# Optimization experiments

Hardware: AMD Instinct MI355X
Metric: run time of the kernel (lower is better)

## Reference

```python
import jax, jax.numpy as jnp
import numpy as np

N = 50000      # nodes
F_IN = 128     # input features
H = 128        # hidden channels
C = 2          # num classes
E = 1600000    # edges
EPS = 1e-5     # BatchNorm eps


def setup_inputs() -> dict:
    key = jax.random.key(0)
    ks = jax.random.split(key, 4)
    x = jax.random.normal(ks[0], (N, F_IN), dtype=jnp.float32)
    edge_index = jax.random.randint(ks[1], (2, E), 0, N, dtype=jnp.int64)
    W1 = jax.random.normal(ks[2], (F_IN, H), dtype=jnp.float32) * 0.05
    W2 = jax.random.normal(ks[3], (H, C), dtype=jnp.float32) * 0.05
    return {
        "x": x, "edge_index": edge_index,
        "bn0_gamma": jnp.ones((F_IN,), jnp.float32), "bn0_beta": jnp.zeros((F_IN,), jnp.float32),
        "bn0_mean": jnp.zeros((F_IN,), jnp.float32), "bn0_var": jnp.ones((F_IN,), jnp.float32),
        "W1": W1, "b1": jnp.zeros((H,), jnp.float32),
        "bn1_gamma": jnp.ones((H,), jnp.float32), "bn1_beta": jnp.zeros((H,), jnp.float32),
        "bn1_mean": jnp.zeros((H,), jnp.float32), "bn1_var": jnp.ones((H,), jnp.float32),
        "W2": W2, "b2": jnp.zeros((C,), jnp.float32),
    }


def batch_norm_eval(x, gamma, beta, mean, var):
    # BatchNorm over nodes, eval mode: use running stats
    return (x - mean) * jax.lax.rsqrt(var + EPS) * gamma + beta


def gcn_conv(x, edge_index, W, b):
    # GCNConv: x @ W, add self-loops, symmetric deg^{-1/2} normalization, scatter-add
    n = x.shape[0]
    xw = x @ W  # [N, out]
    loop = jnp.arange(n, dtype=edge_index.dtype)
    src = jnp.concatenate([edge_index[0], loop])
    dst = jnp.concatenate([edge_index[1], loop])
    deg = jax.ops.segment_sum(jnp.ones_like(dst, dtype=x.dtype), dst, num_segments=n)
    dinv = jnp.where(deg > 0, jax.lax.rsqrt(jnp.maximum(deg, 1.0)), 0.0)
    norm = dinv[src] * dinv[dst]  # [E+N]
    out = jax.ops.segment_sum(xw[src] * norm[:, None], dst, num_segments=n)
    return out + b


def reference(x, edge_index, bn0_gamma, bn0_beta, bn0_mean, bn0_var,
              W1, b1, bn1_gamma, bn1_beta, bn1_mean, bn1_var, W2, b2):
    # Eval mode: dropout / dropout_edge are identity
    h = batch_norm_eval(x, bn0_gamma, bn0_beta, bn0_mean, bn0_var)
    h = gcn_conv(h, edge_index, W1, b1)
    h = batch_norm_eval(h, bn1_gamma, bn1_beta, bn1_mean, bn1_var)
    h = jax.nn.relu(h)
    return gcn_conv(h, edge_index, W2, b2)
```

## Files before the change

### kernel.cpp

```cpp
#include <hip/hip_runtime.h>

#define EPS 1e-5f
#define CAP 128
#define DR  128
#define NB  391
#define CB  4608
#define GS  16
#define CHUNK 4096

typedef __attribute__((ext_vector_type(8))) short bf16x8;
typedef __attribute__((ext_vector_type(4))) float f32x4;

__device__ __forceinline__ unsigned int f2bf(float f) {
  union { float f; unsigned int u; } v; v.f = f;
  return (v.u + 0x7fffu + ((v.u >> 16) & 1u)) >> 16;
}
__device__ __forceinline__ float bf2f_lo(unsigned int u) {
  union { unsigned int i; float f; } v; v.i = u << 16; return v.f;
}
__device__ __forceinline__ float bf2f_hi(unsigned int u) {
  union { unsigned int i; float f; } v; v.i = u & 0xffff0000u; return v.f;
}

__global__ __launch_bounds__(256) void k_prep0(const float* __restrict__ W1, const float* __restrict__ b1,
                       const float* __restrict__ g0, const float* __restrict__ be0,
                       const float* __restrict__ m0, const float* __restrict__ v0,
                       const float* __restrict__ g1, const float* __restrict__ be1,
                       const float* __restrict__ m1, const float* __restrict__ v1,
                       float* __restrict__ W1p, float* __restrict__ c1,
                       float* __restrict__ s1, float* __restrict__ u1,
                       int* __restrict__ gcur) {
  if (blockIdx.x > 0) {
    int i = (blockIdx.x - 1) * 256 + threadIdx.x;
    if (i < NB * GS) gcur[i] = 0;
    return;
  }
  int j = threadIdx.x;
  if (j >= 128) return;
  float acc = 0.f;
  for (int k = 0; k < 128; ++k) {
    float s0 = g0[k] * rsqrtf(v0[k] + EPS);
    float t0 = be0[k] - m0[k] * s0;
    float w = W1[k * 128 + j];
    W1p[k * 128 + j] = s0 * w;
    acc = fmaf(t0, w, acc);
  }
  c1[j] = acc;
  float s = g1[j] * rsqrtf(v1[j] + EPS);
  s1[j] = s;
  u1[j] = fmaf(b1[j] - m1[j], s, be1[j]);
}

__global__ __launch_bounds__(256) void k_cvtx(const float4* __restrict__ x,
                                              uint2* __restrict__ Xb4,
                                              int n4, int npad4) {
  int i = blockIdx.x * 256 + threadIdx.x;
  if (i >= npad4) return;
  uint2 o = make_uint2(0u, 0u);
  if (i < n4) {
    float4 v = x[i];
    o.x = (f2bf(v.y) << 16) | f2bf(v.x);
    o.y = (f2bf(v.w) << 16) | f2bf(v.z);
  }
  Xb4[i] = o;
}

__global__ __launch_bounds__(256) void k_p1(const int* __restrict__ esrc,
                                            const int* __restrict__ edst,
                                            int* __restrict__ gcur,
                                            uint2* __restrict__ coarse, int e) {
  __shared__ int hist[NB];
  __shared__ int base[NB];
  __shared__ int loff[NB];
  for (int i = threadIdx.x; i < NB; i += 256) { hist[i] = 0; loff[i] = 0; }
  __syncthreads();
  int e0 = blockIdx.x * CHUNK;
  int e1 = min(e0 + CHUNK, e);
  for (int i = e0 + threadIdx.x; i < e1; i += 256)
    atomicAdd(&hist[edst[i] >> 7], 1);
  __syncthreads();
  for (int b = threadIdx.x; b < NB; b += 256) {
    int h = hist[b];
    if (h > 0) base[b] = atomicAdd(&gcur[b * GS], h);
  }
  __syncthreads();
  for (int i = e0 + threadIdx.x; i < e1; i += 256) {
    int d = edst[i], s = esrc[i];
    int b = d >> 7;
    int p = base[b] + atomicAdd(&loff[b], 1);
    if (p < CB) coarse[(size_t)b * CB + p] = make_uint2((uint)s, (uint)d);
  }
}

__global__ __launch_bounds__(256) void k_p2(const int* __restrict__ gcur,
                                            const uint2* __restrict__ coarse,
                                            int* __restrict__ slot,
                                            int* __restrict__ wcnt,
                                            float* __restrict__ dinv, int n) {
  __shared__ int lcnt[DR];
  __shared__ int nqs[DR];
  __shared__ int lslot[DR * CAP];
  for (int i = threadIdx.x; i < DR; i += 256) lcnt[i] = 0;
  for (int q = threadIdx.x; q < DR * CAP; q += 256) lslot[q] = n;
  __syncthreads();
  int cb = blockIdx.x;
  int cnt = gcur[cb * GS]; if (cnt > CB) cnt = CB;
  const uint2* src = coarse + (size_t)cb * CB;
  for (int i = threadIdx.x; i < cnt; i += 256) {
    uint2 pr = src[i];
    int ld = (int)(pr.y & 127u);
    int pos = atomicAdd(&lcnt[ld], 1);
    if (pos < CAP) lslot[ld * CAP + pos] = (int)pr.x;
  }
  __syncthreads();
  int dbase = cb * DR;
  for (int ld = threadIdx.x; ld < DR; ld += 256) {
    int c = min(lcnt[ld], CAP);
    nqs[ld] = (c + 3) >> 2;
    int d = dbase + ld;
    if (d < n) {
      wcnt[d] = c;
      dinv[d] = rsqrtf((float)c + 1.0f);
    }
  }
  __syncthreads();
  const int4* lslot4 = (const int4*)lslot;
  int4* slot4 = (int4*)slot;
  for (int idx = threadIdx.x; idx < DR * 32; idx += 256) {
    int ld = idx >> 5, qi = idx & 31;
    if (qi < nqs[ld]) slot4[(size_t)cb * (DR * 32) + idx] = lslot4[idx];
  }
}

__global__ __launch_bounds__(256) void k_gemm1m(const unsigned short* __restrict__ Xb,
                                                const float* __restrict__ W1p,
                                                const float* __restrict__ c1,
                                                const float* __restrict__ dinv,
                                                unsigned short* __restrict__ xsb, int n) {
  __shared__ short wsw[32 * 64 * 8];
  __shared__ float c1s[128];
  const int tid = threadIdx.x;
  for (int idx = tid; idx < 128 * 32; idx += 256) {
    int k = idx >> 5, n4 = (idx & 31) * 4;
    float4 w = ((const float4*)W1p)[idx];
    int c = k >> 5, j = k & 7, lq2 = (k >> 3) & 3;
    float wv[4] = {w.x, w.y, w.z, w.w};
#pragma unroll
    for (int m = 0; m < 4; ++m) {
      int col = n4 + m;
      int t = col >> 4, li = col & 15;
      int l = lq2 * 16 + li;
      wsw[(((c << 3) + t) * 64 + l) * 8 + j] = (short)f2bf(wv[m]);
    }
  }
  if (tid < 128) c1s[tid] = c1[tid];
  if (blockIdx.x == 0 && tid < 16)
    ((uint4*)xsb)[(size_t)n * 16 + tid] = make_uint4(0, 0, 0, 0);
  __syncthreads();
  const int wave = tid >> 6, lane = tid & 63;
  const int r0 = blockIdx.x * 64 + wave * 16;
  const int lr = lane & 15, lq = lane >> 4;
  const bf16x8* a_base = (const bf16x8*)(Xb + (size_t)(r0 + lr) * 128);
  f32x4 acc[8];
#pragma unroll
  for (int t = 0; t < 8; ++t) acc[t] = (f32x4){0.f, 0.f, 0.f, 0.f};
#pragma unroll
  for (int c = 0; c < 4; ++c) {
    bf16x8 a = a_base[c * 4 + lq];
    const bf16x8* bbase = (const bf16x8*)wsw + (c * 8) * 64 + lane;
#pragma unroll
    for (int t = 0; t < 8; ++t) {
      bf16x8 b = bbase[t * 64];
      acc[t] = __builtin_amdgcn_mfma_f32_16x16x32_bf16(a, b, acc[t], 0, 0, 0);
    }
  }
#pragma unroll
  for (int reg = 0; reg < 4; ++reg) {
    int row = r0 + lq * 4 + reg;
    if (row < n) {
      float dd = dinv[row];
      unsigned short* orow = xsb + (size_t)row * 128 + lr;
#pragma unroll
      for (int t = 0; t < 8; ++t) {
        float v = (acc[t][reg] + c1s[t * 16 + lr]) * dd;
        orow[t * 16] = (unsigned short)f2bf(v);
      }
    }
  }
}

__global__ __launch_bounds__(256) void k_gather1(const int* __restrict__ wcnt,
                                                 const int* __restrict__ slot,
                                                 const uint4* __restrict__ xs4,
                                                 const float* __restrict__ dinv,
                                                 const float* __restrict__ s1,
                                                 const float* __restrict__ u1,
                                                 const float* __restrict__ W2,
                                                 float* __restrict__ xs2, int n) {
  int wave = threadIdx.x >> 6, lane = threadIdx.x & 63;
  int d = blockIdx.x * 4 + wave;
  if (d >= n) return;
  int sub = lane >> 4, cl = lane & 15;
  int cnt = wcnt[d];
  int nq = (cnt + 3) >> 2;
  const int* slotd = slot + ((size_t)d << 7);
  float a0 = 0.f, a1 = 0.f, a2 = 0.f, a3 = 0.f, a4 = 0.f, a5 = 0.f, a6 = 0.f, a7 = 0.f;
#define ACC(R) { a0 += bf2f_lo(R.x); a1 += bf2f_hi(R.x); a2 += bf2f_lo(R.y); a3 += bf2f_hi(R.y); \
                 a4 += bf2f_lo(R.z); a5 += bf2f_hi(R.z); a6 += bf2f_lo(R.w); a7 += bf2f_hi(R.w); }
  int q = 0;
  for (; q + 1 < nq; q += 2) {
    int i0 = slotd[q * 4 + sub];
    int i1 = slotd[q * 4 + 4 + sub];
    uint4 r0 = xs4[(size_t)i0 * 16 + cl];
    uint4 r1 = xs4[(size_t)i1 * 16 + cl];
    ACC(r0); ACC(r1);
  }
  if (q < nq) {
    int i0 = slotd[q * 4 + sub];
    uint4 r0 = xs4[(size_t)i0 * 16 + cl];
    ACC(r0);
  }
#define FOLD(OFF) { a0 += __shfl_xor(a0, OFF); a1 += __shfl_xor(a1, OFF); \
                    a2 += __shfl_xor(a2, OFF); a3 += __shfl_xor(a3, OFF); \
                    a4 += __shfl_xor(a4, OFF); a5 += __shfl_xor(a5, OFF); \
                    a6 += __shfl_xor(a6, OFF); a7 += __shfl_xor(a7, OFF); }
  FOLD(16); FOLD(32);
  uint4 sr = xs4[(size_t)d * 16 + cl];
  ACC(sr);
#undef ACC
#undef FOLD
  float dd = dinv[d];
  float4 sA = ((const float4*)s1)[cl * 2], sB = ((const float4*)s1)[cl * 2 + 1];
  float4 uA = ((const float4*)u1)[cl * 2], uB = ((const float4*)u1)[cl * 2 + 1];
  float h0 = fmaxf(fmaf(a0 * dd, sA.x, uA.x), 0.f);
  float h1 = fmaxf(fmaf(a1 * dd, sA.y, uA.y), 0.f);
  float h2 = fmaxf(fmaf(a2 * dd, sA.z, uA.z), 0.f);
  float h3 = fmaxf(fmaf(a3 * dd, sA.w, uA.w), 0.f);
  float h4 = fmaxf(fmaf(a4 * dd, sB.x, uB.x), 0.f);
  float h5 = fmaxf(fmaf(a5 * dd, sB.y, uB.y), 0.f);
  float h6 = fmaxf(fmaf(a6 * dd, sB.z, uB.z), 0.f);
  float h7 = fmaxf(fmaf(a7 * dd, sB.w, uB.w), 0.f);
  float4 wA = ((const float4*)W2)[cl * 4 + 0];
  float4 wB = ((const float4*)W2)[cl * 4 + 1];
  float4 wC = ((const float4*)W2)[cl * 4 + 2];
  float4 wD = ((const float4*)W2)[cl * 4 + 3];
  float p0 = h0 * wA.x + h1 * wA.z + h2 * wB.x + h3 * wB.z
           + h4 * wC.x + h5 * wC.z + h6 * wD.x + h7 * wD.z;
  float p1 = h0 * wA.y + h1 * wA.w + h2 * wB.y + h3 * wB.w
           + h4 * wC.y + h5 * wC.w + h6 * wD.y + h7 * wD.w;
  for (int off = 1; off < 16; off <<= 1) {
    p0 += __shfl_xor(p0, off);
    p1 += __shfl_xor(p1, off);
  }
  if (lane == 0) ((float2*)xs2)[d] = make_float2(p0 * dd, p1 * dd);
}

__global__ __launch_bounds__(256) void k_gather2(const int* __restrict__ wcnt,
                                                 const int* __restrict__ slot,
                                                 const float* __restrict__ xs2,
                                                 const float* __restrict__ dinv,
                                                 const float* __restrict__ b2,
                                                 float* __restrict__ out, int n) {
  int wave = threadIdx.x >> 6, lane = threadIdx.x & 63;
  int d = blockIdx.x * 4 + wave;
  if (d >= n) return;
  int cnt = wcnt[d];
  const int* slotd = slot + ((size_t)d << 7);
  float p0 = 0.f, p1 = 0.f;
  for (int k = lane; k < cnt; k += 64) {
    int s = slotd[k];
    float2 v = ((const float2*)xs2)[s];
    p0 += v.x; p1 += v.y;
  }
  for (int off = 32; off > 0; off >>= 1) {
    p0 += __shfl_down(p0, off);
    p1 += __shfl_down(p1, off);
  }
  if (lane == 0) {
    float dd = dinv[d];
    float2 self = ((const float2*)xs2)[d];
    out[d * 2 + 0] = fmaf(dd, p0 + self.x, b2[0]);
    out[d * 2 + 1] = fmaf(dd, p1 + self.y, b2[1]);
  }
}

extern "C" void kernel_launch(void* const* d_in, const int* in_sizes, int n_in,
                              void* d_out, int out_size, void* d_ws, size_t ws_size,
                              hipStream_t stream) {
  const float* x   = (const float*)d_in[0];
  const int*   ei  = (const int*)d_in[1];
  const float* g0  = (const float*)d_in[2];
  const float* be0 = (const float*)d_in[3];
  const float* m0  = (const float*)d_in[4];
  const float* v0  = (const float*)d_in[5];
  const float* W1  = (const float*)d_in[6];
  const float* b1  = (const float*)d_in[7];
  const float* g1  = (const float*)d_in[8];
  const float* be1 = (const float*)d_in[9];
  const float* m1  = (const float*)d_in[10];
  const float* v1  = (const float*)d_in[11];
  const float* W2  = (const float*)d_in[12];
  const float* b2  = (const float*)d_in[13];
  float* out = (float*)d_out;

  const int n = in_sizes[0] / 128;
  const int e = in_sizes[1] / 2;
  const int* esrc = ei;
  const int* edst = ei + e;
  const int npad = ((n + 63) / 64) * 64;

  int*   gcur   = (int*)d_ws;
  uint2* coarse = (uint2*)(gcur + 6272);
  int*   slot   = (int*)(coarse + (size_t)NB * CB);
  int*   wcnt   = slot + (size_t)n * CAP;
  float* dinv   = (float*)(wcnt + n);
  float* W1p    = dinv + n;
  float* c1     = W1p + 128 * 128;
  float* s1     = c1 + 128;
  float* u1     = s1 + 128;
  float* xs2    = u1 + 128;
  unsigned short* Xb = (unsigned short*)(xs2 + (size_t)n * 2);
  unsigned short* xsb = (unsigned short*)coarse;

  k_prep0<<<1 + (NB * GS + 255) / 256, 256, 0, stream>>>(W1, b1, g0, be0, m0, v0, g1, be1, m1, v1,
                                                         W1p, c1, s1, u1, gcur);
  k_cvtx<<<(npad * 32 + 255) / 256, 256, 0, stream>>>((const float4*)x, (uint2*)Xb,
                                                      n * 32, npad * 32);
  k_p1<<<(e + CHUNK - 1) / CHUNK, 256, 0, stream>>>(esrc, edst, gcur, coarse, e);
  k_p2<<<NB, 256, 0, stream>>>(gcur, coarse, slot, wcnt, dinv, n);
  k_gemm1m<<<npad / 64, 256, 0, stream>>>(Xb, W1p, c1, dinv, xsb, n);
  k_gather1<<<(n + 3) / 4, 256, 0, stream>>>(wcnt, slot, (const uint4*)xsb, dinv, s1, u1, W2, xs2, n);
  k_gather2<<<(n + 3) / 4, 256, 0, stream>>>(wcnt, slot, xs2, dinv, b2, out, n);
}
```

Before: 243.2 us.

## Pack edge/slot indices to 16-bit, fuse prep kernels, preswizzle W1 once

```diff
diff --git a/kernel.cpp b/kernel.cpp
--- a/kernel.cpp
+++ b/kernel.cpp
@@ -7,6 +7,7 @@
 #define CB  4608
 #define GS  16
 #define CHUNK 4096
+#define GZB ((NB * GS + 255) / 256)
 
 typedef __attribute__((ext_vector_type(8))) short bf16x8;
 typedef __attribute__((ext_vector_type(4))) float f32x4;
@@ -22,39 +23,51 @@
   union { unsigned int i; float f; } v; v.i = u & 0xffff0000u; return v.f;
 }
 
-__global__ __launch_bounds__(256) void k_prep0(const float* __restrict__ W1, const float* __restrict__ b1,
-                       const float* __restrict__ g0, const float* __restrict__ be0,
-                       const float* __restrict__ m0, const float* __restrict__ v0,
-                       const float* __restrict__ g1, const float* __restrict__ be1,
-                       const float* __restrict__ m1, const float* __restrict__ v1,
-                       float* __restrict__ W1p, float* __restrict__ c1,
-                       float* __restrict__ s1, float* __restrict__ u1,
-                       int* __restrict__ gcur) {
-  if (blockIdx.x > 0) {
-    int i = (blockIdx.x - 1) * 256 + threadIdx.x;
+__global__ __launch_bounds__(256) void k_prep_all(
+    const float* __restrict__ W1, const float* __restrict__ b1,
+    const float* __restrict__ g0, const float* __restrict__ be0,
+    const float* __restrict__ m0, const float* __restrict__ v0,
+    const float* __restrict__ g1, const float* __restrict__ be1,
+    const float* __restrict__ m1, const float* __restrict__ v1,
+    const float4* __restrict__ x,
+    unsigned short* __restrict__ Wb, float* __restrict__ c1,
+    float* __restrict__ s1, float* __restrict__ u1,
+    int* __restrict__ gcur, uint2* __restrict__ Xb4, int n4, int npad4) {
+  int bid = blockIdx.x;
+  int tid = threadIdx.x;
+  if (bid == 0) {
+    __shared__ float s0s[128], t0s[128];
+    if (tid < 128) {
+      float s0 = g0[tid] * rsqrtf(v0[tid] + EPS);
+      s0s[tid] = s0;
+      t0s[tid] = be0[tid] - m0[tid] * s0;
+      float s = g1[tid] * rsqrtf(v1[tid] + EPS);
+      s1[tid] = s;
+      u1[tid] = fmaf(b1[tid] - m1[tid], s, be1[tid]);
+    }
+    __syncthreads();
+    if (tid < 128) {
+      float acc = 0.f;
+      for (int k = 0; k < 128; ++k) acc = fmaf(t0s[k], W1[k * 128 + tid], acc);
+      c1[tid] = acc;
+    }
+    for (int idx = tid; idx < 16384; idx += 256) {
+      int k = idx >> 7, col = idx & 127;
+      float w = W1[idx] * s0s[k];
+      int c = k >> 5, j = k & 7, lq2 = (k >> 3) & 3;
+      int t = col >> 4, li = col & 15;
+      Wb[(((c * 8 + t) * 64) + lq2 * 16 + li) * 8 + j] = (unsigned short)f2bf(w);
+    }
+    return;
+  }
+  bid -= 1;
+  if (bid < GZB) {
+    int i = bid * 256 + tid;
     if (i < NB * GS) gcur[i] = 0;
     return;
   }
-  int j = threadIdx.x;
-  if (j >= 128) return;
-  float acc = 0.f;
-  for (int k = 0; k < 128; ++k) {
-    float s0 = g0[k] * rsqrtf(v0[k] + EPS);
-    float t0 = be0[k] - m0[k] * s0;
-    float w = W1[k * 128 + j];
-    W1p[k * 128 + j] = s0 * w;
-    acc = fmaf(t0, w, acc);
-  }
-  c1[j] = acc;
-  float s = g1[j] * rsqrtf(v1[j] + EPS);
-  s1[j] = s;
-  u1[j] = fmaf(b1[j] - m1[j], s, be1[j]);
-}
-
-__global__ __launch_bounds__(256) void k_cvtx(const float4* __restrict__ x,
-                                              uint2* __restrict__ Xb4,
-                                              int n4, int npad4) {
-  int i = blockIdx.x * 256 + threadIdx.x;
+  bid -= GZB;
+  int i = bid * 256 + tid;
   if (i >= npad4) return;
   uint2 o = make_uint2(0u, 0u);
   if (i < n4) {
@@ -68,7 +81,7 @@
 __global__ __launch_bounds__(256) void k_p1(const int* __restrict__ esrc,
                                             const int* __restrict__ edst,
                                             int* __restrict__ gcur,
-                                            uint2* __restrict__ coarse, int e) {
+                                            unsigned int* __restrict__ coarse, int e) {
   __shared__ int hist[NB];
   __shared__ int base[NB];
   __shared__ int loff[NB];
@@ -79,7 +92,9 @@
   for (int i = e0 + threadIdx.x; i < e1; i += 256)
     atomicAdd(&hist[edst[i] >> 7], 1);
   __syncthreads();
-  for (int b = threadIdx.x; b < NB; b += 256) {
+  int rot = blockIdx.x % NB;
+  for (int bb = threadIdx.x; bb < NB; bb += 256) {
+    int b = bb + rot; if (b >= NB) b -= NB;
     int h = hist[b];
     if (h > 0) base[b] = atomicAdd(&gcur[b * GS], h);
   }
@@ -88,35 +103,36 @@
     int d = edst[i], s = esrc[i];
     int b = d >> 7;
     int p = base[b] + atomicAdd(&loff[b], 1);
-    if (p < CB) coarse[(size_t)b * CB + p] = make_uint2((uint)s, (uint)d);
+    if (p < CB) coarse[(size_t)b * CB + p] = ((unsigned int)(d & 127) << 16) | (unsigned int)s;
   }
 }
 
 __global__ __launch_bounds__(256) void k_p2(const int* __restrict__ gcur,
-                                            const uint2* __restrict__ coarse,
-                                            int* __restrict__ slot,
+                                            const unsigned int* __restrict__ coarse,
+                                            unsigned short* __restrict__ slot,
                                             int* __restrict__ wcnt,
                                             float* __restrict__ dinv, int n) {
   __shared__ int lcnt[DR];
-  __shared__ int nqs[DR];
-  __shared__ int lslot[DR * CAP];
+  __shared__ int nqr[DR];
+  __shared__ unsigned short lslot[DR * CAP];
   for (int i = threadIdx.x; i < DR; i += 256) lcnt[i] = 0;
-  for (int q = threadIdx.x; q < DR * CAP; q += 256) lslot[q] = n;
+  unsigned int padpat = ((unsigned int)n << 16) | (unsigned int)n;
+  for (int q = threadIdx.x; q < DR * CAP / 2; q += 256) ((unsigned int*)lslot)[q] = padpat;
   __syncthreads();
   int cb = blockIdx.x;
   int cnt = gcur[cb * GS]; if (cnt > CB) cnt = CB;
-  const uint2* src = coarse + (size_t)cb * CB;
+  const unsigned int* src = coarse + (size_t)cb * CB;
   for (int i = threadIdx.x; i < cnt; i += 256) {
-    uint2 pr = src[i];
-    int ld = (int)(pr.y & 127u);
+    unsigned int v = src[i];
+    int ld = (int)(v >> 16);
     int pos = atomicAdd(&lcnt[ld], 1);
-    if (pos < CAP) lslot[ld * CAP + pos] = (int)pr.x;
+    if (pos < CAP) lslot[ld * CAP + pos] = (unsigned short)(v & 0xffffu);
   }
   __syncthreads();
   int dbase = cb * DR;
   for (int ld = threadIdx.x; ld < DR; ld += 256) {
     int c = min(lcnt[ld], CAP);
-    nqs[ld] = (c + 3) >> 2;
+    nqr[ld] = ((((c + 3) >> 2) + 3) & ~3);
     int d = dbase + ld;
     if (d < n) {
       wcnt[d] = c;
@@ -124,53 +140,36 @@
     }
   }
   __syncthreads();
-  const int4* lslot4 = (const int4*)lslot;
-  int4* slot4 = (int4*)slot;
+  const uint2* ls8 = (const uint2*)lslot;
+  uint2* s8 = (uint2*)slot;
   for (int idx = threadIdx.x; idx < DR * 32; idx += 256) {
     int ld = idx >> 5, qi = idx & 31;
-    if (qi < nqs[ld]) slot4[(size_t)cb * (DR * 32) + idx] = lslot4[idx];
+    if (qi < nqr[ld] && dbase + ld < n) s8[(size_t)cb * (DR * 32) + idx] = ls8[idx];
   }
 }
 
 __global__ __launch_bounds__(256) void k_gemm1m(const unsigned short* __restrict__ Xb,
-                                                const float* __restrict__ W1p,
+                                                const unsigned short* __restrict__ Wb,
                                                 const float* __restrict__ c1,
                                                 const float* __restrict__ dinv,
                                                 unsigned short* __restrict__ xsb, int n) {
-  __shared__ short wsw[32 * 64 * 8];
-  __shared__ float c1s[128];
   const int tid = threadIdx.x;
-  for (int idx = tid; idx < 128 * 32; idx += 256) {
-    int k = idx >> 5, n4 = (idx & 31) * 4;
-    float4 w = ((const float4*)W1p)[idx];
-    int c = k >> 5, j = k & 7, lq2 = (k >> 3) & 3;
-    float wv[4] = {w.x, w.y, w.z, w.w};
-#pragma unroll
-    for (int m = 0; m < 4; ++m) {
-      int col = n4 + m;
-      int t = col >> 4, li = col & 15;
-      int l = lq2 * 16 + li;
-      wsw[(((c << 3) + t) * 64 + l) * 8 + j] = (short)f2bf(wv[m]);
-    }
-  }
-  if (tid < 128) c1s[tid] = c1[tid];
   if (blockIdx.x == 0 && tid < 16)
     ((uint4*)xsb)[(size_t)n * 16 + tid] = make_uint4(0, 0, 0, 0);
-  __syncthreads();
   const int wave = tid >> 6, lane = tid & 63;
   const int r0 = blockIdx.x * 64 + wave * 16;
   const int lr = lane & 15, lq = lane >> 4;
   const bf16x8* a_base = (const bf16x8*)(Xb + (size_t)(r0 + lr) * 128);
+  const bf16x8* wb = (const bf16x8*)Wb;
   f32x4 acc[8];
 #pragma unroll
   for (int t = 0; t < 8; ++t) acc[t] = (f32x4){0.f, 0.f, 0.f, 0.f};
 #pragma unroll
   for (int c = 0; c < 4; ++c) {
     bf16x8 a = a_base[c * 4 + lq];
-    const bf16x8* bbase = (const bf16x8*)wsw + (c * 8) * 64 + lane;
 #pragma unroll
     for (int t = 0; t < 8; ++t) {
-      bf16x8 b = bbase[t * 64];
+      bf16x8 b = wb[(c * 8 + t) * 64 + lane];
       acc[t] = __builtin_amdgcn_mfma_f32_16x16x32_bf16(a, b, acc[t], 0, 0, 0);
     }
   }
@@ -182,7 +181,7 @@
       unsigned short* orow = xsb + (size_t)row * 128 + lr;
 #pragma unroll
       for (int t = 0; t < 8; ++t) {
-        float v = (acc[t][reg] + c1s[t * 16 + lr]) * dd;
+        float v = (acc[t][reg] + c1[t * 16 + lr]) * dd;
         orow[t * 16] = (unsigned short)f2bf(v);
       }
     }
@@ -190,7 +189,7 @@
 }
 
 __global__ __launch_bounds__(256) void k_gather1(const int* __restrict__ wcnt,
-                                                 const int* __restrict__ slot,
+                                                 const unsigned short* __restrict__ slot,
                                                  const uint4* __restrict__ xs4,
                                                  const float* __restrict__ dinv,
                                                  const float* __restrict__ s1,
@@ -202,23 +201,21 @@
   if (d >= n) return;
   int sub = lane >> 4, cl = lane & 15;
   int cnt = wcnt[d];
-  int nq = (cnt + 3) >> 2;
-  const int* slotd = slot + ((size_t)d << 7);
+  int nq4 = ((((cnt + 3) >> 2) + 3) & ~3);
+  const unsigned short* slotd = slot + ((size_t)d << 7);
   float a0 = 0.f, a1 = 0.f, a2 = 0.f, a3 = 0.f, a4 = 0.f, a5 = 0.f, a6 = 0.f, a7 = 0.f;
 #define ACC(R) { a0 += bf2f_lo(R.x); a1 += bf2f_hi(R.x); a2 += bf2f_lo(R.y); a3 += bf2f_hi(R.y); \
                  a4 += bf2f_lo(R.z); a5 += bf2f_hi(R.z); a6 += bf2f_lo(R.w); a7 += bf2f_hi(R.w); }
-  int q = 0;
-  for (; q + 1 < nq; q += 2) {
-    int i0 = slotd[q * 4 + sub];
-    int i1 = slotd[q * 4 + 4 + sub];
+  for (int q = 0; q < nq4; q += 4) {
+    int i0 = slotd[(q + 0) * 4 + sub];
+    int i1 = slotd[(q + 1) * 4 + sub];
+    int i2 = slotd[(q + 2) * 4 + sub];
+    int i3 = slotd[(q + 3) * 4 + sub];
     uint4 r0 = xs4[(size_t)i0 * 16 + cl];
     uint4 r1 = xs4[(size_t)i1 * 16 + cl];
-    ACC(r0); ACC(r1);
-  }
-  if (q < nq) {
-    int i0 = slotd[q * 4 + sub];
-    uint4 r0 = xs4[(size_t)i0 * 16 + cl];
-    ACC(r0);
+    uint4 r2 = xs4[(size_t)i2 * 16 + cl];
+    uint4 r3 = xs4[(size_t)i3 * 16 + cl];
+    ACC(r0); ACC(r1); ACC(r2); ACC(r3);
   }
 #define FOLD(OFF) { a0 += __shfl_xor(a0, OFF); a1 += __shfl_xor(a1, OFF); \
                     a2 += __shfl_xor(a2, OFF); a3 += __shfl_xor(a3, OFF); \
@@ -256,7 +253,7 @@
 }
 
 __global__ __launch_bounds__(256) void k_gather2(const int* __restrict__ wcnt,
-                                                 const int* __restrict__ slot,
+                                                 const unsigned short* __restrict__ slot,
                                                  const float* __restrict__ xs2,
                                                  const float* __restrict__ dinv,
                                                  const float* __restrict__ b2,
@@ -265,7 +262,7 @@
   int d = blockIdx.x * 4 + wave;
   if (d >= n) return;
   int cnt = wcnt[d];
-  const int* slotd = slot + ((size_t)d << 7);
+  const unsigned short* slotd = slot + ((size_t)d << 7);
   float p0 = 0.f, p1 = 0.f;
   for (int k = lane; k < cnt; k += 64) {
     int s = slotd[k];
@@ -309,26 +306,26 @@
   const int* edst = ei + e;
   const int npad = ((n + 63) / 64) * 64;
 
-  int*   gcur   = (int*)d_ws;
-  uint2* coarse = (uint2*)(gcur + 6272);
-  int*   slot   = (int*)(coarse + (size_t)NB * CB);
-  int*   wcnt   = slot + (size_t)n * CAP;
-  float* dinv   = (float*)(wcnt + n);
-  float* W1p    = dinv + n;
-  float* c1     = W1p + 128 * 128;
-  float* s1     = c1 + 128;
-  float* u1     = s1 + 128;
-  float* xs2    = u1 + 128;
-  unsigned short* Xb = (unsigned short*)(xs2 + (size_t)n * 2);
-  unsigned short* xsb = (unsigned short*)coarse;
-
-  k_prep0<<<1 + (NB * GS + 255) / 256, 256, 0, stream>>>(W1, b1, g0, be0, m0, v0, g1, be1, m1, v1,
-                                                         W1p, c1, s1, u1, gcur);
-  k_cvtx<<<(npad * 32 + 255) / 256, 256, 0, stream>>>((const float4*)x, (uint2*)Xb,
-                                                      n * 32, npad * 32);
+  int*            gcur   = (int*)d_ws;
+  unsigned int*   coarse = (unsigned int*)(gcur + 6272);
+  unsigned short* slot   = (unsigned short*)(coarse + (size_t)NB * CB);
+  int*            wcnt   = (int*)(slot + (size_t)n * CAP);
+  float*          dinv   = (float*)(wcnt + n);
+  unsigned short* Wb     = (unsigned short*)(dinv + n);
+  float*          c1     = (float*)(Wb + 16384);
+  float*          s1     = c1 + 128;
+  float*          u1     = s1 + 128;
+  float*          xs2    = u1 + 128;
+  unsigned short* Xb     = (unsigned short*)(xs2 + (size_t)n * 2);
+  unsigned short* xsb    = Xb + (size_t)npad * 128;
+
+  const int cvb = (npad * 32 + 255) / 256;
+  k_prep_all<<<1 + GZB + cvb, 256, 0, stream>>>(W1, b1, g0, be0, m0, v0, g1, be1, m1, v1,
+                                                (const float4*)x, Wb, c1, s1, u1, gcur,
+                                                (uint2*)Xb, n * 32, npad * 32);
   k_p1<<<(e + CHUNK - 1) / CHUNK, 256, 0, stream>>>(esrc, edst, gcur, coarse, e);
   k_p2<<<NB, 256, 0, stream>>>(gcur, coarse, slot, wcnt, dinv, n);
-  k_gemm1m<<<npad / 64, 256, 0, stream>>>(Xb, W1p, c1, dinv, xsb, n);
+  k_gemm1m<<<npad / 64, 256, 0, stream>>>(Xb, Wb, c1, dinv, xsb, n);
   k_gather1<<<(n + 3) / 4, 256, 0, stream>>>(wcnt, slot, (const uint4*)xsb, dinv, s1, u1, W2, xs2, n);
   k_gather2<<<(n + 3) / 4, 256, 0, stream>>>(wcnt, slot, xs2, dinv, b2, out, n);
 }
```

Measured after the change: 218.4 us. 10.2% less time.
